# Performance work log

Hardware: AMD Instinct MI355X
Metric: run time of the kernel (lower is better)

Reference implementation:

```python
import jax, jax.numpy as jnp
import numpy as np

MAX_DIFF = 0.5


def setup_inputs() -> dict:
    key = jax.random.key(0)
    actions = jax.random.normal(key, (4096, 256, 64), dtype=jnp.float32)
    return {"actions": actions}


def reference(actions):
    # actions: [B, T, A]
    # diffs along time, clamped, then reconstruct via prefix sum from actions[:, 0]
    diffs = jnp.clip(jnp.diff(actions, axis=1), -MAX_DIFF, MAX_DIFF)  # [B, T-1, A]
    rest = actions[:, :1, :] + jnp.cumsum(diffs, axis=1)              # [B, T-1, A]
    return jnp.concatenate([actions[:, :1, :], rest], axis=1)         # [B, T, A]
```

## Files before the change

### kernel.cpp

```cpp
#include <hip/hip_runtime.h>
#include <hip/hip_bf16.h>


__global__ __launch_bounds__(256) void smoothness_kernel(
    const float* __restrict__ in, float* __restrict__ out) {
    constexpr int T = 256;
    constexpr int A4 = 16;

    const int tid = blockIdx.x * blockDim.x + threadIdx.x;
    const int b   = tid >> 4;
    const int a4  = tid & 15;

    const size_t base = (size_t)b * T * A4 + a4;
    const float4* __restrict__ ip = (const float4*)in + base;
    float4* __restrict__ op       = (float4*)out + base;

    float4 prev = ip[0];
    float4 acc  = prev;
    op[0] = acc;

    #pragma unroll 8
    for (int t = 1; t < T; ++t) {
        float4 cur = ip[t * A4];
        float dx = fminf(fmaxf(cur.x - prev.x, -0.5f), 0.5f);
        float dy = fminf(fmaxf(cur.y - prev.y, -0.5f), 0.5f);
        float dz = fminf(fmaxf(cur.z - prev.z, -0.5f), 0.5f);
        float dw = fminf(fmaxf(cur.w - prev.w, -0.5f), 0.5f);
        acc.x += dx; acc.y += dy; acc.z += dz; acc.w += dw;
        op[t * A4] = acc;
        prev = cur;
    }
}

extern "C" void kernel_launch(void* const* d_in, const int* in_sizes, int n_in,
                              void* d_out, int out_size, void* d_ws, size_t ws_size,
                              hipStream_t stream) {
    const float* in = (const float*)d_in[0];
    float* out = (float*)d_out;

    constexpr int B = 4096, A = 64;
    const int threads = B * (A / 4);
    const int block = 256;
    const int grid = threads / block;

    smoothness_kernel<<<grid, block, 0, stream>>>(in, out);
}
```

Before: 433.5 us.

## Split time scan into segments with block-level LDS offset combine

Each block now handles one batch row, and its 256 threads split the 256 timesteps into 16 segments of 16. Each thread does a local clipped-diff scan in registers, the segment totals are combined through LDS, and the thread then adds its prefix offset before storing. The old kernel ran each thread serially over all 256 timesteps with a dependent chain, so each thread's memory access stayed serialized. The new layout raises memory-level parallelism and shortens that chain, at the cost of extra loads at segment boundaries, a barrier, and register pressure from 16 float4 values.

```diff
diff --git a/kernel.cpp b/kernel.cpp
--- a/kernel.cpp
+++ b/kernel.cpp
@@ -2,33 +2,61 @@
 #include <hip/hip_bf16.h>
 
 
-__global__ __launch_bounds__(256) void smoothness_kernel(
+__device__ __forceinline__ float clip05(float d) {
+    return fminf(fmaxf(d, -0.5f), 0.5f);
+}
+
+__global__ __launch_bounds__(256) void smooth_scan(
     const float* __restrict__ in, float* __restrict__ out) {
-    constexpr int T = 256;
-    constexpr int A4 = 16;
+    constexpr int T    = 256;
+    constexpr int A4   = 16;
+    constexpr int SEG  = 16;
+    constexpr int NSEG = 16;
 
-    const int tid = blockIdx.x * blockDim.x + threadIdx.x;
-    const int b   = tid >> 4;
-    const int a4  = tid & 15;
+    __shared__ float4 lds_x0[A4];
+    __shared__ float4 lds_tot[NSEG][A4];
 
-    const size_t base = (size_t)b * T * A4 + a4;
+    const int b   = blockIdx.x;
+    const int a4  = threadIdx.x & (A4 - 1);
+    const int seg = threadIdx.x >> 4;
+
+    const size_t base = (size_t)b * T * A4 + (size_t)seg * SEG * A4 + a4;
     const float4* __restrict__ ip = (const float4*)in + base;
-    float4* __restrict__ op       = (float4*)out + base;
+    float4*       __restrict__ op = (float4*)out + base;
 
-    float4 prev = ip[0];
-    float4 acc  = prev;
-    op[0] = acc;
+    float4 v[SEG];
+#pragma unroll
+    for (int i = 0; i < SEG; ++i) v[i] = ip[i * A4];
 
-    #pragma unroll 8
-    for (int t = 1; t < T; ++t) {
-        float4 cur = ip[t * A4];
-        float dx = fminf(fmaxf(cur.x - prev.x, -0.5f), 0.5f);
-        float dy = fminf(fmaxf(cur.y - prev.y, -0.5f), 0.5f);
-        float dz = fminf(fmaxf(cur.z - prev.z, -0.5f), 0.5f);
-        float dw = fminf(fmaxf(cur.w - prev.w, -0.5f), 0.5f);
-        acc.x += dx; acc.y += dy; acc.z += dz; acc.w += dw;
-        op[t * A4] = acc;
+    float4 prev = (seg != 0) ? ip[-A4] : v[0];
+
+    if (seg == 0) lds_x0[a4] = v[0];
+
+    float4 run = make_float4(0.f, 0.f, 0.f, 0.f);
+#pragma unroll
+    for (int i = 0; i < SEG; ++i) {
+        const float4 cur = v[i];
+        run.x += clip05(cur.x - prev.x);
+        run.y += clip05(cur.y - prev.y);
+        run.z += clip05(cur.z - prev.z);
+        run.w += clip05(cur.w - prev.w);
         prev = cur;
+        v[i] = run;
+    }
+
+    lds_tot[seg][a4] = run;
+    __syncthreads();
+
+    float4 off = lds_x0[a4];
+    for (int s = 0; s < seg; ++s) {
+        const float4 t = lds_tot[s][a4];
+        off.x += t.x; off.y += t.y; off.z += t.z; off.w += t.w;
+    }
+
+#pragma unroll
+    for (int i = 0; i < SEG; ++i) {
+        const float4 r = v[i];
+        op[i * A4] = make_float4(off.x + r.x, off.y + r.y, off.z + r.z, off.w + r.w);
     }
 }
 
@@ -38,10 +66,6 @@
     const float* in = (const float*)d_in[0];
     float* out = (float*)d_out;
 
-    constexpr int B = 4096, A = 64;
-    const int threads = B * (A / 4);
-    const int block = 256;
-    const int grid = threads / block;
-
-    smoothness_kernel<<<grid, block, 0, stream>>>(in, out);
+    constexpr int B = 4096;
+    smooth_scan<<<B, 256, 0, stream>>>(in, out);
 }
```

Measured after the change: 435.3 us. No clear change (+0.4%).
